# Kernel tuning notes

Measured on AMD Instinct MI355X. Metric: run time of the kernel, lower is better.

## Reference

```python
import jax, jax.numpy as jnp
import numpy as np

N = 50000        # nodes
E = 1_600_000    # edges (avg degree 32)
IN = 512         # in_size
OUT = 512        # out_size
H = 8            # num_heads
D = OUT // H     # head_dim = 64


def setup_inputs() -> dict:
    key = jax.random.key(0)
    ks = jax.random.split(key, 9)
    w_scale = 0.02
    h = jax.random.normal(ks[0], (N, IN), dtype=jnp.float32)
    Wq = jax.random.normal(ks[1], (IN, OUT), dtype=jnp.float32) * w_scale
    bq = jnp.zeros((OUT,), dtype=jnp.float32)
    Wk = jax.random.normal(ks[2], (IN, OUT), dtype=jnp.float32) * w_scale
    bk = jnp.zeros((OUT,), dtype=jnp.float32)
    Wv = jax.random.normal(ks[3], (IN, OUT), dtype=jnp.float32) * w_scale
    bv = jnp.zeros((OUT,), dtype=jnp.float32)
    row = jax.random.randint(ks[4], (E,), 0, N)  # dst node of each edge
    col = jax.random.randint(ks[5], (E,), 0, N)  # src node of each edge
    return {"h": h, "Wq": Wq, "bq": bq, "Wk": Wk, "bk": bk, "Wv": Wv, "bv": bv, "row": row, "col": col}


def reference(h, Wq, bq, Wk, bk, Wv, bv, row, col):
    n = h.shape[0]
    scaling = D ** -0.5
    # prep_qkv: Linear projections, reshape to [N, head_dim, num_heads], scale q
    q = ((h @ Wq) + bq).reshape(n, D, H) * scaling
    k = ((h @ Wk) + bk).reshape(n, D, H)
    v = ((h @ Wv) + bv).reshape(n, D, H)
    # bsddmm: per-nonzero batched dot product, scores[e,h] = <q[row[e],:,h], k[col[e],:,h]>
    scores = jnp.einsum('edh,edh->eh', q[row], k[col])  # [E, H]
    # sparse row-wise softmax over neighbors of each dst node
    m = jax.lax.stop_gradient(jax.ops.segment_max(scores, row, num_segments=n))  # [N, H]
    ex = jnp.exp(scores - m[row])                                                # [E, H]
    denom = jax.ops.segment_sum(ex, row, num_segments=n)                         # [N, H]
    attn = ex / denom[row]                                                       # [E, H]
    # bspmm: out[i,d,h] = sum_{e: row[e]=i} attn[e,h] * v[col[e],d,h]
    out = jax.ops.segment_sum(attn[:, None, :] * v[col], row, num_segments=n)    # [N, D, H]
    return out
```

## Files before the change

kernel.cpp:

```cpp
#include <hip/hip_runtime.h>
#include <hip/hip_bf16.h>
#include <math.h>


#define IN_DIM 512
#define OUT_DIM 512
#define NHEAD 8
#define HDIM 64
#define BM 128
#define BN 128
#define BK 32

typedef short bf16x8 __attribute__((ext_vector_type(8)));
typedef float f32x4 __attribute__((ext_vector_type(4)));
typedef unsigned short ushort8_t __attribute__((ext_vector_type(8)));

__device__ __forceinline__ unsigned short f2bf(float f) {
  union { float f; unsigned int u; } v; v.f = f;
  unsigned int u = v.u;
  u = (u + 0x7FFF + ((u >> 16) & 1)) >> 16;
  return (unsigned short)u;
}
__device__ __forceinline__ float bf2f(unsigned short s) {
  union { unsigned int u; float f; } v; v.u = ((unsigned int)s) << 16;
  return v.f;
}
__device__ __forceinline__ void gload_lds16(const void* g, void* l) {
  __builtin_amdgcn_global_load_lds(
      (const __attribute__((address_space(1))) unsigned int*)g,
      (__attribute__((address_space(3))) unsigned int*)l, 16, 0, 0);
}

__global__ __launch_bounds__(256) void convert_h(const float* __restrict__ Hm,
                                                 unsigned short* __restrict__ hb,
                                                 int Nn) {
  const size_t base = ((size_t)blockIdx.x * blockDim.x + threadIdx.x) * 8;
  const int row = (int)(base >> 9);
  ushort8_t o = {0,0,0,0,0,0,0,0};
  if (row < Nn) {
    const float4 a = *(const float4*)(Hm + base);
    const float4 b = *(const float4*)(Hm + base + 4);
    o[0]=f2bf(a.x); o[1]=f2bf(a.y); o[2]=f2bf(a.z); o[3]=f2bf(a.w);
    o[4]=f2bf(b.x); o[5]=f2bf(b.y); o[6]=f2bf(b.z); o[7]=f2bf(b.w);
  }
  *(ushort8_t*)(hb + base) = o;
}

__global__ __launch_bounds__(256) void convert_w(const float* __restrict__ Wq,
                                                 const float* __restrict__ Wk,
                                                 const float* __restrict__ Wv,
                                                 unsigned short* __restrict__ Wt) {
  __shared__ unsigned short tile[64][72];
  const int mat = blockIdx.z;
  const float* W = (mat == 0) ? Wq : (mat == 1) ? Wk : Wv;
  const int k0 = blockIdx.x * 64, n0 = blockIdx.y * 64;
  const int tid = threadIdx.x;
  const int r = tid >> 2, cb = (tid & 3) * 16;
  #pragma unroll
  for (int x = 0; x < 16; x += 4) {
    const float4 f = *(const float4*)(W + (size_t)(k0 + r) * OUT_DIM + n0 + cb + x);
    tile[cb + x + 0][r] = f2bf(f.x);
    tile[cb + x + 1][r] = f2bf(f.y);
    tile[cb + x + 2][r] = f2bf(f.z);
    tile[cb + x + 3][r] = f2bf(f.w);
  }
  __syncthreads();
  ushort8_t o1, o2;
  #pragma unroll
  for (int x = 0; x < 8; ++x) { o1[x] = tile[r][cb + x]; o2[x] = tile[r][cb + 8 + x]; }
  const int n = n0 + r;
  const int np = ((n & 7) << 6) | (n >> 3);
  unsigned short* dst = Wt + (size_t)(mat * 512 + np) * IN_DIM + k0 + cb;
  *(ushort8_t*)(dst) = o1;
  *(ushort8_t*)(dst + 8) = o2;
}

__global__ __launch_bounds__(256, 2) void qkv_gemm_mfma(
    const unsigned short* __restrict__ hb,
    const unsigned short* __restrict__ Wt,
    const float* __restrict__ bq, const float* __restrict__ bk, const float* __restrict__ bv,
    unsigned short* __restrict__ qTb, unsigned short* __restrict__ kTb,
    unsigned short* __restrict__ vTb, int Nn) {
  __shared__ __align__(16) unsigned short As[BM * BK];
  __shared__ __align__(16) unsigned short Bs[BN * BK];
  const int tid = threadIdx.x;
  const int l = tid & 63;
  const int w = tid >> 6;
  const int wr = w >> 1, wc = w & 1;
  const int row0 = blockIdx.x * BM;
  const int col0 = blockIdx.y * BN;

  const int kcl = tid & 3;
  const int rl0 = tid >> 2;

  for (int mat = 0; mat < 3; ++mat) {
    const unsigned short* Bsrc = Wt + (size_t)(mat * 512 + col0) * IN_DIM;
    f32x4 acc[4][4];
    const f32x4 zero = {0.f, 0.f, 0.f, 0.f};
    #pragma unroll
    for (int m = 0; m < 4; ++m)
      #pragma unroll
      for (int n = 0; n < 4; ++n) acc[m][n] = zero;

    for (int k0 = 0; k0 < IN_DIM; k0 += BK) {
      __syncthreads();
      #pragma unroll
      for (int t = 0; t < 2; ++t) {
        const int rl = rl0 + t * 64;
        const int kk = (kcl ^ ((rl >> 1) & 3)) * 8;
        gload_lds16(hb + (size_t)(row0 + rl) * IN_DIM + k0 + kk,
                    (char*)As + t * 4096 + w * 1024);
        gload_lds16(Bsrc + (size_t)rl * IN_DIM + k0 + kk,
                    (char*)Bs + t * 4096 + w * 1024);
      }
      __syncthreads();
      bf16x8 af[4], bfr[4];
      #pragma unroll
      for (int m = 0; m < 4; ++m) {
        const int row = wr * 64 + m * 16 + (l & 15);
        const int kc = (l >> 4) ^ ((row >> 1) & 3);
        af[m] = *(const bf16x8*)&As[row * BK + kc * 8];
      }
      #pragma unroll
      for (int n = 0; n < 4; ++n) {
        const int row = wc * 64 + n * 16 + (l & 15);
        const int kc = (l >> 4) ^ ((row >> 1) & 3);
        bfr[n] = *(const bf16x8*)&Bs[row * BK + kc * 8];
      }
      #pragma unroll
      for (int m = 0; m < 4; ++m)
        #pragma unroll
        for (int n = 0; n < 4; ++n)
          acc[m][n] = __builtin_amdgcn_mfma_f32_16x16x32_bf16(af[m], bfr[n], acc[m][n], 0, 0, 0);
    }

    const float scale = (mat == 0) ? 0.125f : 1.0f;
    const float* bias = (mat == 0) ? bq : (mat == 1) ? bk : bv;
    unsigned short* dst = (mat == 0) ? qTb : (mat == 1) ? kTb : vTb;
    #pragma unroll
    for (int n = 0; n < 4; ++n) {
      const int cc = col0 + wc * 64 + n * 16 + (l & 15);
      const int o = ((cc & 63) << 3) | (cc >> 6);
      const float bsv = bias[o];
      #pragma unroll
      for (int m = 0; m < 4; ++m) {
        #pragma unroll
        for (int j = 0; j < 4; ++j) {
          const int r = row0 + wr * 64 + m * 16 + (l >> 4) * 4 + j;
          if (r < Nn) dst[(size_t)r * OUT_DIM + cc] = f2bf((acc[m][n][j] + bsv) * scale);
        }
      }
    }
  }
}

__global__ void hist_kernel(const int* __restrict__ row, int* __restrict__ counts, int E_) {
  const int i = blockIdx.x * blockDim.x + threadIdx.x;
  if (i < E_) atomicAdd(&counts[row[i]], 1);
}

__global__ __launch_bounds__(1024) void scan_kernel(const int* __restrict__ counts,
                                                    int* __restrict__ offsets,
                                                    int* __restrict__ cursor, int n) {
  __shared__ int lds[1024];
  __shared__ int running_s;
  const int t = threadIdx.x;
  if (t == 0) running_s = 0;
  __syncthreads();
  for (int base = 0; base < n; base += 1024) {
    const int i = base + t;
    const int c = (i < n) ? counts[i] : 0;
    lds[t] = c;
    __syncthreads();
    int val = c;
    for (int off = 1; off < 1024; off <<= 1) {
      const int add = (t >= off) ? lds[t - off] : 0;
      __syncthreads();
      val += add;
      lds[t] = val;
      __syncthreads();
    }
    const int running = running_s;
    if (i < n) { const int ex = running + val - c; offsets[i] = ex; cursor[i] = ex; }
    __syncthreads();
    if (t == 1023) running_s = running + val;
    __syncthreads();
  }
  if (t == 0) offsets[n] = running_s;
}

__global__ void scatter_kernel(const int* __restrict__ row, const int* __restrict__ col,
                               int* __restrict__ cursor, int* __restrict__ colsorted, int E_) {
  const int i = blockIdx.x * blockDim.x + threadIdx.x;
  if (i < E_) {
    const int pos = atomicAdd(&cursor[row[i]], 1);
    colsorted[pos] = col[i];
  }
}

__global__ __launch_bounds__(256) void bsddmm_node(
    const unsigned short* __restrict__ qb, const unsigned short* __restrict__ kb,
    const int* __restrict__ colsorted, const int* __restrict__ offsets,
    float* __restrict__ scores, float* __restrict__ nodemax, int Nn) {
  const int wid = (int)((blockIdx.x * (size_t)blockDim.x + threadIdx.x) >> 6);
  if (wid >= Nn) return;
  const int l = threadIdx.x & 63;
  const int hh = l >> 3, j = l & 7;
  const int start = offsets[wid], end = offsets[wid + 1];
  if (start == end) return;

  const size_t loff = (size_t)l * 8;
  const ushort8_t q8 = *(const ushort8_t*)(qb + (size_t)wid * OUT_DIM + loff);
  float qf[8];
  #pragma unroll
  for (int x = 0; x < 8; ++x) qf[x] = bf2f(q8[x]);

  float m_run = -1e30f;

  for (int base = start; base < end; base += 64) {
    const int cnt = min(64, end - base);
    const int myc = (l < cnt) ? colsorted[base + l] : 0;
    int u = 0;
    for (; u + 4 <= cnt; u += 4) {
      const int c0 = __shfl(myc, u + 0);
      const int c1 = __shfl(myc, u + 1);
      const int c2 = __shfl(myc, u + 2);
      const int c3 = __shfl(myc, u + 3);
      const ushort8_t ka = *(const ushort8_t*)(kb + (size_t)c0 * OUT_DIM + loff);
      const ushort8_t kb1 = *(const ushort8_t*)(kb + (size_t)c1 * OUT_DIM + loff);
      const ushort8_t kc = *(const ushort8_t*)(kb + (size_t)c2 * OUT_DIM + loff);
      const ushort8_t kd = *(const ushort8_t*)(kb + (size_t)c3 * OUT_DIM + loff);
      float s0 = 0.f, s1 = 0.f, s2 = 0.f, s3 = 0.f;
      #pragma unroll
      for (int x = 0; x < 8; ++x) {
        s0 = fmaf(qf[x], bf2f(ka[x]), s0);
        s1 = fmaf(qf[x], bf2f(kb1[x]), s1);
        s2 = fmaf(qf[x], bf2f(kc[x]), s2);
        s3 = fmaf(qf[x], bf2f(kd[x]), s3);
      }
      s0 += __shfl_xor(s0, 1); s0 += __shfl_xor(s0, 2); s0 += __shfl_xor(s0, 4);
      s1 += __shfl_xor(s1, 1); s1 += __shfl_xor(s1, 2); s1 += __shfl_xor(s1, 4);
      s2 += __shfl_xor(s2, 1); s2 += __shfl_xor(s2, 2); s2 += __shfl_xor(s2, 4);
      s3 += __shfl_xor(s3, 1); s3 += __shfl_xor(s3, 2); s3 += __shfl_xor(s3, 4);
      m_run = fmaxf(m_run, fmaxf(fmaxf(s0, s1), fmaxf(s2, s3)));
      if (j == 0) {
        scores[(size_t)(base + u + 0) * NHEAD + hh] = s0;
        scores[(size_t)(base + u + 1) * NHEAD + hh] = s1;
        scores[(size_t)(base + u + 2) * NHEAD + hh] = s2;
        scores[(size_t)(base + u + 3) * NHEAD + hh] = s3;
      }
    }
    for (; u < cnt; ++u) {
      const int c = __shfl(myc, u);
      const ushort8_t kv = *(const ushort8_t*)(kb + (size_t)c * OUT_DIM + loff);
      float s = 0.f;
      #pragma unroll
      for (int x = 0; x < 8; ++x) s = fmaf(qf[x], bf2f(kv[x]), s);
      s += __shfl_xor(s, 1); s += __shfl_xor(s, 2); s += __shfl_xor(s, 4);
      m_run = fmaxf(m_run, s);
      if (j == 0) scores[(size_t)(base + u) * NHEAD + hh] = s;
    }
  }
  if (j == 0) nodemax[(size_t)wid * NHEAD + hh] = m_run;
}

__device__ __forceinline__ float sel8(const float v[8], int idx) {
  float r = v[0];
  r = (idx == 1) ? v[1] : r;
  r = (idx == 2) ? v[2] : r;
  r = (idx == 3) ? v[3] : r;
  r = (idx == 4) ? v[4] : r;
  r = (idx == 5) ? v[5] : r;
  r = (idx == 6) ? v[6] : r;
  r = (idx == 7) ? v[7] : r;
  return r;
}

__global__ __launch_bounds__(256) void softmax_spmm_kernel(
    const float* __restrict__ scores, const float* __restrict__ nodemax,
    const unsigned short* __restrict__ vb,
    const int* __restrict__ colsorted, const int* __restrict__ offsets,
    float* __restrict__ out, int Nn) {
  const int wid = (int)((blockIdx.x * (size_t)blockDim.x + threadIdx.x) >> 6);
  if (wid >= Nn) return;
  const int l = threadIdx.x & 63;
  const int hh = l >> 3;
  const int dg = (l & 7) * 8;
  const int start = offsets[wid], end = offsets[wid + 1];

  if (start == end) {
    #pragma unroll
    for (int x = 0; x < 8; ++x)
      out[(size_t)wid * OUT_DIM + (size_t)(dg + x) * NHEAD + hh] = 0.f;
    return;
  }

  const float4 ma = *(const float4*)(nodemax + (size_t)wid * NHEAD);
  const float4 mb = *(const float4*)(nodemax + (size_t)wid * NHEAD + 4);
  const float m[8] = {ma.x, ma.y, ma.z, ma.w, mb.x, mb.y, mb.z, mb.w};

  float dsum[8];
  #pragma unroll
  for (int x = 0; x < 8; ++x) dsum[x] = 0.f;
  for (int s = start + l; s < end; s += 64) {
    const float4 a = *(const float4*)(scores + (size_t)s * NHEAD);
    const float4 b = *(const float4*)(scores + (size_t)s * NHEAD + 4);
    dsum[0] += __expf(a.x - m[0]); dsum[1] += __expf(a.y - m[1]);
    dsum[2] += __expf(a.z - m[2]); dsum[3] += __expf(a.w - m[3]);
    dsum[4] += __expf(b.x - m[4]); dsum[5] += __expf(b.y - m[5]);
    dsum[6] += __expf(b.z - m[6]); dsum[7] += __expf(b.w - m[7]);
  }
  #pragma unroll
  for (int off = 1; off < 64; off <<= 1) {
    #pragma unroll
    for (int x = 0; x < 8; ++x) dsum[x] += __shfl_xor(dsum[x], off);
  }

  const float mh  = sel8(m, hh);
  const float inv = 1.0f / sel8(dsum, hh);

  float acc[8];
  #pragma unroll
  for (int x = 0; x < 8; ++x) acc[x] = 0.f;
  const size_t loff = (size_t)l * 8;
  for (int base = start; base < end; base += 64) {
    const int cnt = min(64, end - base);
    const int myc = (l < cnt) ? colsorted[base + l] : 0;
    int u = 0;
    for (; u + 4 <= cnt; u += 4) {
      const int c0 = __shfl(myc, u + 0);
      const int c1 = __shfl(myc, u + 1);
      const int c2 = __shfl(myc, u + 2);
      const int c3 = __shfl(myc, u + 3);
      const float e0 = __expf(scores[(size_t)(base + u + 0) * NHEAD + hh] - mh);
      const float e1 = __expf(scores[(size_t)(base + u + 1) * NHEAD + hh] - mh);
      const float e2 = __expf(scores[(size_t)(base + u + 2) * NHEAD + hh] - mh);
      const float e3 = __expf(scores[(size_t)(base + u + 3) * NHEAD + hh] - mh);
      const ushort8_t va = *(const ushort8_t*)(vb + (size_t)c0 * OUT_DIM + loff);
      const ushort8_t vb1 = *(const ushort8_t*)(vb + (size_t)c1 * OUT_DIM + loff);
      const ushort8_t vc = *(const ushort8_t*)(vb + (size_t)c2 * OUT_DIM + loff);
      const ushort8_t vd = *(const ushort8_t*)(vb + (size_t)c3 * OUT_DIM + loff);
      #pragma unroll
      for (int x = 0; x < 8; ++x) {
        acc[x] = fmaf(e0, bf2f(va[x]), acc[x]);
        acc[x] = fmaf(e1, bf2f(vb1[x]), acc[x]);
        acc[x] = fmaf(e2, bf2f(vc[x]), acc[x]);
        acc[x] = fmaf(e3, bf2f(vd[x]), acc[x]);
      }
    }
    for (; u < cnt; ++u) {
      const int c = __shfl(myc, u);
      const float e = __expf(scores[(size_t)(base + u) * NHEAD + hh] - mh);
      const ushort8_t vv = *(const ushort8_t*)(vb + (size_t)c * OUT_DIM + loff);
      #pragma unroll
      for (int x = 0; x < 8; ++x) acc[x] = fmaf(e, bf2f(vv[x]), acc[x]);
    }
  }
  #pragma unroll
  for (int x = 0; x < 8; ++x)
    out[(size_t)wid * OUT_DIM + (size_t)(dg + x) * NHEAD + hh] = acc[x] * inv;
}

extern "C" void kernel_launch(void* const* d_in, const int* in_sizes, int n_in,
                              void* d_out, int out_size, void* d_ws, size_t ws_size,
                              hipStream_t stream) {
  const float* Hm = (const float*)d_in[0];
  const float* Wq = (const float*)d_in[1];
  const float* bq = (const float*)d_in[2];
  const float* Wk = (const float*)d_in[3];
  const float* bk = (const float*)d_in[4];
  const float* Wv = (const float*)d_in[5];
  const float* bv = (const float*)d_in[6];
  const int* row  = (const int*)d_in[7];
  const int* col  = (const int*)d_in[8];
  float* out = (float*)d_out;

  const int Nn = in_sizes[0] / IN_DIM;
  const int E  = in_sizes[7];
  const int mtiles = (Nn + BM - 1) / BM;
  const int Mpad = mtiles * BM;

  unsigned short* hb  = (unsigned short*)d_ws;
  unsigned short* Wt  = hb + (size_t)Mpad * IN_DIM;
  unsigned short* qTb = Wt + (size_t)3 * 512 * IN_DIM;
  unsigned short* kTb = qTb + (size_t)Nn * OUT_DIM;
  unsigned short* vTb = kTb + (size_t)Nn * OUT_DIM;
  float* scores   = (float*)(vTb + (size_t)Nn * OUT_DIM);
  float* nodemax  = scores + (size_t)E * NHEAD;
  int* counts     = (int*)(nodemax + (size_t)Nn * NHEAD);
  int* offsets    = counts + Nn;
  int* cursor     = offsets + Nn + 1;
  int* colsorted  = cursor + Nn;

  hipMemsetAsync(counts, 0, (size_t)Nn * sizeof(int), stream);
  hist_kernel<<<(E + 255) / 256, 256, 0, stream>>>(row, counts, E);
  scan_kernel<<<1, 1024, 0, stream>>>(counts, offsets, cursor, Nn);
  scatter_kernel<<<(E + 255) / 256, 256, 0, stream>>>(row, col, cursor, colsorted, E);

  const int hblocks = (int)(((size_t)Mpad * IN_DIM / 8 + 255) / 256);
  convert_h<<<hblocks, 256, 0, stream>>>(Hm, hb, Nn);
  convert_w<<<dim3(8, 8, 3), 256, 0, stream>>>(Wq, Wk, Wv, Wt);

  qkv_gemm_mfma<<<dim3(mtiles, 4), 256, 0, stream>>>(hb, Wt, bq, bk, bv,
                                                     qTb, kTb, vTb, Nn);

  const size_t node_threads = (size_t)Nn * 64;
  bsddmm_node<<<(int)((node_threads + 255) / 256), 256, 0, stream>>>(
      qTb, kTb, colsorted, offsets, scores, nodemax, Nn);

  softmax_spmm_kernel<<<(int)((node_threads + 255) / 256), 256, 0, stream>>>(
      scores, nodemax, vTb, colsorted, offsets, out, Nn);
}
```

Measured before the change: 1.129 ms.

## Fuse SDDMM, softmax and SpMM per node with LDS scores; parallelize scan

Merges the score computation, the row softmax and the value aggregation into one kernel. Each wavefront keeps its node's scores in shared memory when the degree is at most 128, so the global scores and nodemax round trips go away, and each score is exponentiated once. Nodes with higher degree fall back to a global scratch path. The single-block sequential prefix scan is replaced by a three-kernel multi-block scan, which removes a serial bottleneck at the cost of two extra launches. The fused kernel uses 16KB of LDS per block, which may limit occupancy.

```diff
diff --git a/kernel.cpp b/kernel.cpp
--- a/kernel.cpp
+++ b/kernel.cpp
@@ -10,6 +10,7 @@
 #define BM 128
 #define BN 128
 #define BK 32
+#define SEGCAP 128
 
 typedef short bf16x8 __attribute__((ext_vector_type(8)));
 typedef float f32x4 __attribute__((ext_vector_type(4)));
@@ -159,34 +160,59 @@
   if (i < E_) atomicAdd(&counts[row[i]], 1);
 }
 
-__global__ __launch_bounds__(1024) void scan_kernel(const int* __restrict__ counts,
-                                                    int* __restrict__ offsets,
-                                                    int* __restrict__ cursor, int n) {
+__global__ __launch_bounds__(256) void scan_partial(const int* __restrict__ counts,
+                                                    int* __restrict__ bsums, int n) {
+  __shared__ int red[256];
+  const int t = threadIdx.x;
+  const int i = blockIdx.x * 256 + t;
+  red[t] = (i < n) ? counts[i] : 0;
+  __syncthreads();
+  #pragma unroll
+  for (int off = 128; off > 0; off >>= 1) {
+    if (t < off) red[t] += red[t + off];
+    __syncthreads();
+  }
+  if (t == 0) bsums[blockIdx.x] = red[0];
+}
+
+__global__ __launch_bounds__(1024) void scan_bsums(int* __restrict__ bsums, int nb) {
   __shared__ int lds[1024];
-  __shared__ int running_s;
   const int t = threadIdx.x;
-  if (t == 0) running_s = 0;
+  const int v = (t < nb) ? bsums[t] : 0;
+  lds[t] = v;
   __syncthreads();
-  for (int base = 0; base < n; base += 1024) {
-    const int i = base + t;
-    const int c = (i < n) ? counts[i] : 0;
-    lds[t] = c;
+  for (int off = 1; off < 1024; off <<= 1) {
+    const int add = (t >= off) ? lds[t - off] : 0;
     __syncthreads();
-    int val = c;
-    for (int off = 1; off < 1024; off <<= 1) {
-      const int add = (t >= off) ? lds[t - off] : 0;
-      __syncthreads();
-      val += add;
-      lds[t] = val;
-      __syncthreads();
-    }
-    const int running = running_s;
-    if (i < n) { const int ex = running + val - c; offsets[i] = ex; cursor[i] = ex; }
+    lds[t] += add;
     __syncthreads();
-    if (t == 1023) running_s = running + val;
+  }
+  if (t < nb) bsums[t] = lds[t] - v;
+}
+
+__global__ __launch_bounds__(256) void scan_final(const int* __restrict__ counts,
+                                                  const int* __restrict__ bsums,
+                                                  int* __restrict__ offsets,
+                                                  int* __restrict__ cursor,
+                                                  int n, int E_) {
+  __shared__ int lds[256];
+  const int t = threadIdx.x;
+  const int i = blockIdx.x * 256 + t;
+  const int c = (i < n) ? counts[i] : 0;
+  lds[t] = c;
+  __syncthreads();
+  for (int off = 1; off < 256; off <<= 1) {
+    const int add = (t >= off) ? lds[t - off] : 0;
     __syncthreads();
-  }
-  if (t == 0) offsets[n] = running_s;
+    lds[t] += add;
+    __syncthreads();
+  }
+  if (i < n) {
+    const int ex = lds[t] - c + bsums[blockIdx.x];
+    offsets[i] = ex;
+    cursor[i] = ex;
+  }
+  if (blockIdx.x == 0 && t == 0) offsets[n] = E_;
 }
 
 __global__ void scatter_kernel(const int* __restrict__ row, const int* __restrict__ col,
@@ -198,164 +224,173 @@
   }
 }
 
-__global__ __launch_bounds__(256) void bsddmm_node(
+__global__ __launch_bounds__(256) void fused_attn(
     const unsigned short* __restrict__ qb, const unsigned short* __restrict__ kb,
+    const unsigned short* __restrict__ vb,
     const int* __restrict__ colsorted, const int* __restrict__ offsets,
-    float* __restrict__ scores, float* __restrict__ nodemax, int Nn) {
+    float* __restrict__ gscores,
+    float* __restrict__ out, int Nn) {
+  __shared__ float slds_all[4][SEGCAP * NHEAD];
   const int wid = (int)((blockIdx.x * (size_t)blockDim.x + threadIdx.x) >> 6);
   if (wid >= Nn) return;
   const int l = threadIdx.x & 63;
   const int hh = l >> 3, j = l & 7;
   const int start = offsets[wid], end = offsets[wid + 1];
-  if (start == end) return;
-
+  const int seg = end - start;
   const size_t loff = (size_t)l * 8;
-  const ushort8_t q8 = *(const ushort8_t*)(qb + (size_t)wid * OUT_DIM + loff);
-  float qf[8];
-  #pragma unroll
-  for (int x = 0; x < 8; ++x) qf[x] = bf2f(q8[x]);
-
-  float m_run = -1e30f;
-
-  for (int base = start; base < end; base += 64) {
-    const int cnt = min(64, end - base);
-    const int myc = (l < cnt) ? colsorted[base + l] : 0;
-    int u = 0;
-    for (; u + 4 <= cnt; u += 4) {
-      const int c0 = __shfl(myc, u + 0);
-      const int c1 = __shfl(myc, u + 1);
-      const int c2 = __shfl(myc, u + 2);
-      const int c3 = __shfl(myc, u + 3);
-      const ushort8_t ka = *(const ushort8_t*)(kb + (size_t)c0 * OUT_DIM + loff);
-      const ushort8_t kb1 = *(const ushort8_t*)(kb + (size_t)c1 * OUT_DIM + loff);
-      const ushort8_t kc = *(const ushort8_t*)(kb + (size_t)c2 * OUT_DIM + loff);
-      const ushort8_t kd = *(const ushort8_t*)(kb + (size_t)c3 * OUT_DIM + loff);
-      float s0 = 0.f, s1 = 0.f, s2 = 0.f, s3 = 0.f;
-      #pragma unroll
-      for (int x = 0; x < 8; ++x) {
-        s0 = fmaf(qf[x], bf2f(ka[x]), s0);
-        s1 = fmaf(qf[x], bf2f(kb1[x]), s1);
-        s2 = fmaf(qf[x], bf2f(kc[x]), s2);
-        s3 = fmaf(qf[x], bf2f(kd[x]), s3);
-      }
-      s0 += __shfl_xor(s0, 1); s0 += __shfl_xor(s0, 2); s0 += __shfl_xor(s0, 4);
-      s1 += __shfl_xor(s1, 1); s1 += __shfl_xor(s1, 2); s1 += __shfl_xor(s1, 4);
-      s2 += __shfl_xor(s2, 1); s2 += __shfl_xor(s2, 2); s2 += __shfl_xor(s2, 4);
-      s3 += __shfl_xor(s3, 1); s3 += __shfl_xor(s3, 2); s3 += __shfl_xor(s3, 4);
-      m_run = fmaxf(m_run, fmaxf(fmaxf(s0, s1), fmaxf(s2, s3)));
-      if (j == 0) {
-        scores[(size_t)(base + u + 0) * NHEAD + hh] = s0;
-        scores[(size_t)(base + u + 1) * NHEAD + hh] = s1;
-        scores[(size_t)(base + u + 2) * NHEAD + hh] = s2;
-        scores[(size_t)(base + u + 3) * NHEAD + hh] = s3;
-      }
-    }
-    for (; u < cnt; ++u) {
-      const int c = __shfl(myc, u);
-      const ushort8_t kv = *(const ushort8_t*)(kb + (size_t)c * OUT_DIM + loff);
-      float s = 0.f;
-      #pragma unroll
-      for (int x = 0; x < 8; ++x) s = fmaf(qf[x], bf2f(kv[x]), s);
-      s += __shfl_xor(s, 1); s += __shfl_xor(s, 2); s += __shfl_xor(s, 4);
-      m_run = fmaxf(m_run, s);
-      if (j == 0) scores[(size_t)(base + u) * NHEAD + hh] = s;
-    }
-  }
-  if (j == 0) nodemax[(size_t)wid * NHEAD + hh] = m_run;
-}
-
-__device__ __forceinline__ float sel8(const float v[8], int idx) {
-  float r = v[0];
-  r = (idx == 1) ? v[1] : r;
-  r = (idx == 2) ? v[2] : r;
-  r = (idx == 3) ? v[3] : r;
-  r = (idx == 4) ? v[4] : r;
-  r = (idx == 5) ? v[5] : r;
-  r = (idx == 6) ? v[6] : r;
-  r = (idx == 7) ? v[7] : r;
-  return r;
-}
-
-__global__ __launch_bounds__(256) void softmax_spmm_kernel(
-    const float* __restrict__ scores, const float* __restrict__ nodemax,
-    const unsigned short* __restrict__ vb,
-    const int* __restrict__ colsorted, const int* __restrict__ offsets,
-    float* __restrict__ out, int Nn) {
-  const int wid = (int)((blockIdx.x * (size_t)blockDim.x + threadIdx.x) >> 6);
-  if (wid >= Nn) return;
-  const int l = threadIdx.x & 63;
-  const int hh = l >> 3;
   const int dg = (l & 7) * 8;
-  const int start = offsets[wid], end = offsets[wid + 1];
-
-  if (start == end) {
-    #pragma unroll
-    for (int x = 0; x < 8; ++x)
-      out[(size_t)wid * OUT_DIM + (size_t)(dg + x) * NHEAD + hh] = 0.f;
-    return;
-  }
-
-  const float4 ma = *(const float4*)(nodemax + (size_t)wid * NHEAD);
-  const float4 mb = *(const float4*)(nodemax + (size_t)wid * NHEAD + 4);
-  const float m[8] = {ma.x, ma.y, ma.z, ma.w, mb.x, mb.y, mb.z, mb.w};
-
-  float dsum[8];
-  #pragma unroll
-  for (int x = 0; x < 8; ++x) dsum[x] = 0.f;
-  for (int s = start + l; s < end; s += 64) {
-    const float4 a = *(const float4*)(scores + (size_t)s * NHEAD);
-    const float4 b = *(const float4*)(scores + (size_t)s * NHEAD + 4);
-    dsum[0] += __expf(a.x - m[0]); dsum[1] += __expf(a.y - m[1]);
-    dsum[2] += __expf(a.z - m[2]); dsum[3] += __expf(a.w - m[3]);
-    dsum[4] += __expf(b.x - m[4]); dsum[5] += __expf(b.y - m[5]);
-    dsum[6] += __expf(b.z - m[6]); dsum[7] += __expf(b.w - m[7]);
-  }
-  #pragma unroll
-  for (int off = 1; off < 64; off <<= 1) {
-    #pragma unroll
-    for (int x = 0; x < 8; ++x) dsum[x] += __shfl_xor(dsum[x], off);
-  }
-
-  const float mh  = sel8(m, hh);
-  const float inv = 1.0f / sel8(dsum, hh);
 
   float acc[8];
   #pragma unroll
   for (int x = 0; x < 8; ++x) acc[x] = 0.f;
-  const size_t loff = (size_t)l * 8;
-  for (int base = start; base < end; base += 64) {
-    const int cnt = min(64, end - base);
-    const int myc = (l < cnt) ? colsorted[base + l] : 0;
-    int u = 0;
-    for (; u + 4 <= cnt; u += 4) {
-      const int c0 = __shfl(myc, u + 0);
-      const int c1 = __shfl(myc, u + 1);
-      const int c2 = __shfl(myc, u + 2);
-      const int c3 = __shfl(myc, u + 3);
-      const float e0 = __expf(scores[(size_t)(base + u + 0) * NHEAD + hh] - mh);
-      const float e1 = __expf(scores[(size_t)(base + u + 1) * NHEAD + hh] - mh);
-      const float e2 = __expf(scores[(size_t)(base + u + 2) * NHEAD + hh] - mh);
-      const float e3 = __expf(scores[(size_t)(base + u + 3) * NHEAD + hh] - mh);
-      const ushort8_t va = *(const ushort8_t*)(vb + (size_t)c0 * OUT_DIM + loff);
-      const ushort8_t vb1 = *(const ushort8_t*)(vb + (size_t)c1 * OUT_DIM + loff);
-      const ushort8_t vc = *(const ushort8_t*)(vb + (size_t)c2 * OUT_DIM + loff);
-      const ushort8_t vd = *(const ushort8_t*)(vb + (size_t)c3 * OUT_DIM + loff);
-      #pragma unroll
-      for (int x = 0; x < 8; ++x) {
-        acc[x] = fmaf(e0, bf2f(va[x]), acc[x]);
-        acc[x] = fmaf(e1, bf2f(vb1[x]), acc[x]);
-        acc[x] = fmaf(e2, bf2f(vc[x]), acc[x]);
-        acc[x] = fmaf(e3, bf2f(vd[x]), acc[x]);
+  float inv = 0.f;
+
+  if (seg > 0) {
+    const ushort8_t q8 = *(const ushort8_t*)(qb + (size_t)wid * OUT_DIM + loff);
+    float qf[8];
+    #pragma unroll
+    for (int x = 0; x < 8; ++x) qf[x] = bf2f(q8[x]);
+
+    if (seg <= SEGCAP) {
+      float* slds = slds_all[threadIdx.x >> 6];
+      const int myc0 = (l < seg) ? colsorted[start + l] : 0;
+      const int myc1 = (64 + l < seg) ? colsorted[start + 64 + l] : 0;
+      float m_run = -1e30f;
+
+      #pragma unroll
+      for (int chunk = 0; chunk < 2; ++chunk) {
+        const int base = chunk * 64;
+        if (base >= seg) break;
+        const int cnt = min(64, seg - base);
+        const int myc = chunk ? myc1 : myc0;
+        int u = 0;
+        for (; u + 4 <= cnt; u += 4) {
+          const int c0 = __shfl(myc, u + 0);
+          const int c1 = __shfl(myc, u + 1);
+          const int c2 = __shfl(myc, u + 2);
+          const int c3 = __shfl(myc, u + 3);
+          const ushort8_t ka = *(const ushort8_t*)(kb + (size_t)c0 * OUT_DIM + loff);
+          const ushort8_t kb1 = *(const ushort8_t*)(kb + (size_t)c1 * OUT_DIM + loff);
+          const ushort8_t kc = *(const ushort8_t*)(kb + (size_t)c2 * OUT_DIM + loff);
+          const ushort8_t kd = *(const ushort8_t*)(kb + (size_t)c3 * OUT_DIM + loff);
+          float s0 = 0.f, s1 = 0.f, s2 = 0.f, s3 = 0.f;
+          #pragma unroll
+          for (int x = 0; x < 8; ++x) {
+            s0 = fmaf(qf[x], bf2f(ka[x]), s0);
+            s1 = fmaf(qf[x], bf2f(kb1[x]), s1);
+            s2 = fmaf(qf[x], bf2f(kc[x]), s2);
+            s3 = fmaf(qf[x], bf2f(kd[x]), s3);
+          }
+          s0 += __shfl_xor(s0, 1); s0 += __shfl_xor(s0, 2); s0 += __shfl_xor(s0, 4);
+          s1 += __shfl_xor(s1, 1); s1 += __shfl_xor(s1, 2); s1 += __shfl_xor(s1, 4);
+          s2 += __shfl_xor(s2, 1); s2 += __shfl_xor(s2, 2); s2 += __shfl_xor(s2, 4);
+          s3 += __shfl_xor(s3, 1); s3 += __shfl_xor(s3, 2); s3 += __shfl_xor(s3, 4);
+          m_run = fmaxf(m_run, fmaxf(fmaxf(s0, s1), fmaxf(s2, s3)));
+          if (j == 0) {
+            slds[(base + u + 0) * NHEAD + hh] = s0;
+            slds[(base + u + 1) * NHEAD + hh] = s1;
+            slds[(base + u + 2) * NHEAD + hh] = s2;
+            slds[(base + u + 3) * NHEAD + hh] = s3;
+          }
+        }
+        for (; u < cnt; ++u) {
+          const int c = __shfl(myc, u);
+          const ushort8_t kv = *(const ushort8_t*)(kb + (size_t)c * OUT_DIM + loff);
+          float s = 0.f;
+          #pragma unroll
+          for (int x = 0; x < 8; ++x) s = fmaf(qf[x], bf2f(kv[x]), s);
+          s += __shfl_xor(s, 1); s += __shfl_xor(s, 2); s += __shfl_xor(s, 4);
+          m_run = fmaxf(m_run, s);
+          if (j == 0) slds[(base + u) * NHEAD + hh] = s;
+        }
+      }
+      __builtin_amdgcn_wave_barrier();
+
+      float dsum = 0.f;
+      for (int u = j; u < seg; u += 8) {
+        const float ex = __expf(slds[u * NHEAD + hh] - m_run);
+        slds[u * NHEAD + hh] = ex;
+        dsum += ex;
+      }
+      dsum += __shfl_xor(dsum, 1);
+      dsum += __shfl_xor(dsum, 2);
+      dsum += __shfl_xor(dsum, 4);
+      inv = 1.0f / dsum;
+      __builtin_amdgcn_wave_barrier();
+
+      #pragma unroll
+      for (int chunk = 0; chunk < 2; ++chunk) {
+        const int base = chunk * 64;
+        if (base >= seg) break;
+        const int cnt = min(64, seg - base);
+        const int myc = chunk ? myc1 : myc0;
+        int u = 0;
+        for (; u + 4 <= cnt; u += 4) {
+          const int c0 = __shfl(myc, u + 0);
+          const int c1 = __shfl(myc, u + 1);
+          const int c2 = __shfl(myc, u + 2);
+          const int c3 = __shfl(myc, u + 3);
+          const float e0 = slds[(base + u + 0) * NHEAD + hh];
+          const float e1 = slds[(base + u + 1) * NHEAD + hh];
+          const float e2 = slds[(base + u + 2) * NHEAD + hh];
+          const float e3 = slds[(base + u + 3) * NHEAD + hh];
+          const ushort8_t va = *(const ushort8_t*)(vb + (size_t)c0 * OUT_DIM + loff);
+          const ushort8_t vb1 = *(const ushort8_t*)(vb + (size_t)c1 * OUT_DIM + loff);
+          const ushort8_t vc = *(const ushort8_t*)(vb + (size_t)c2 * OUT_DIM + loff);
+          const ushort8_t vd = *(const ushort8_t*)(vb + (size_t)c3 * OUT_DIM + loff);
+          #pragma unroll
+          for (int x = 0; x < 8; ++x) {
+            acc[x] = fmaf(e0, bf2f(va[x]), acc[x]);
+            acc[x] = fmaf(e1, bf2f(vb1[x]), acc[x]);
+            acc[x] = fmaf(e2, bf2f(vc[x]), acc[x]);
+            acc[x] = fmaf(e3, bf2f(vd[x]), acc[x]);
+          }
+        }
+        for (; u < cnt; ++u) {
+          const int c = __shfl(myc, u);
+          const float e = slds[(base + u) * NHEAD + hh];
+          const ushort8_t vv = *(const ushort8_t*)(vb + (size_t)c * OUT_DIM + loff);
+          #pragma unroll
+          for (int x = 0; x < 8; ++x) acc[x] = fmaf(e, bf2f(vv[x]), acc[x]);
+        }
+      }
+    } else {
+      float m_run = -1e30f;
+      for (int base = start; base < end; base += 64) {
+        const int cnt = min(64, end - base);
+        const int myc = (l < cnt) ? colsorted[base + l] : 0;
+        for (int u = 0; u < cnt; ++u) {
+          const int c = __shfl(myc, u);
+          const ushort8_t kv = *(const ushort8_t*)(kb + (size_t)c * OUT_DIM + loff);
+          float s = 0.f;
+          #pragma unroll
+          for (int x = 0; x < 8; ++x) s = fmaf(qf[x], bf2f(kv[x]), s);
+          s += __shfl_xor(s, 1); s += __shfl_xor(s, 2); s += __shfl_xor(s, 4);
+          m_run = fmaxf(m_run, s);
+          if (j == 0) gscores[(size_t)(base + u) * NHEAD + hh] = s;
+        }
+      }
+      float dsum = 0.f;
+      for (int e = start + j; e < end; e += 8)
+        dsum += __expf(gscores[(size_t)e * NHEAD + hh] - m_run);
+      dsum += __shfl_xor(dsum, 1);
+      dsum += __shfl_xor(dsum, 2);
+      dsum += __shfl_xor(dsum, 4);
+      inv = 1.0f / dsum;
+      for (int base = start; base < end; base += 64) {
+        const int cnt = min(64, end - base);
+        const int myc = (l < cnt) ? colsorted[base + l] : 0;
+        for (int u = 0; u < cnt; ++u) {
+          const int c = __shfl(myc, u);
+          const float e = __expf(gscores[(size_t)(base + u) * NHEAD + hh] - m_run);
+          const ushort8_t vv = *(const ushort8_t*)(vb + (size_t)c * OUT_DIM + loff);
+          #pragma unroll
+          for (int x = 0; x < 8; ++x) acc[x] = fmaf(e, bf2f(vv[x]), acc[x]);
+        }
       }
     }
-    for (; u < cnt; ++u) {
-      const int c = __shfl(myc, u);
-      const float e = __expf(scores[(size_t)(base + u) * NHEAD + hh] - mh);
-      const ushort8_t vv = *(const ushort8_t*)(vb + (size_t)c * OUT_DIM + loff);
-      #pragma unroll
-      for (int x = 0; x < 8; ++x) acc[x] = fmaf(e, bf2f(vv[x]), acc[x]);
-    }
-  }
+  }
+
   #pragma unroll
   for (int x = 0; x < 8; ++x)
     out[(size_t)wid * OUT_DIM + (size_t)(dg + x) * NHEAD + hh] = acc[x] * inv;
@@ -379,22 +414,25 @@
   const int E  = in_sizes[7];
   const int mtiles = (Nn + BM - 1) / BM;
   const int Mpad = mtiles * BM;
+  const int nb = (Nn + 255) / 256;
 
   unsigned short* hb  = (unsigned short*)d_ws;
   unsigned short* Wt  = hb + (size_t)Mpad * IN_DIM;
   unsigned short* qTb = Wt + (size_t)3 * 512 * IN_DIM;
   unsigned short* kTb = qTb + (size_t)Nn * OUT_DIM;
   unsigned short* vTb = kTb + (size_t)Nn * OUT_DIM;
-  float* scores   = (float*)(vTb + (size_t)Nn * OUT_DIM);
-  float* nodemax  = scores + (size_t)E * NHEAD;
-  int* counts     = (int*)(nodemax + (size_t)Nn * NHEAD);
+  float* gscores  = (float*)(vTb + (size_t)Nn * OUT_DIM);
+  int* counts     = (int*)(gscores + (size_t)E * NHEAD);
   int* offsets    = counts + Nn;
   int* cursor     = offsets + Nn + 1;
   int* colsorted  = cursor + Nn;
+  int* bsums      = colsorted + E;
 
   hipMemsetAsync(counts, 0, (size_t)Nn * sizeof(int), stream);
   hist_kernel<<<(E + 255) / 256, 256, 0, stream>>>(row, counts, E);
-  scan_kernel<<<1, 1024, 0, stream>>>(counts, offsets, cursor, Nn);
+  scan_partial<<<nb, 256, 0, stream>>>(counts, bsums, Nn);
+  scan_bsums<<<1, 1024, 0, stream>>>(bsums, nb);
+  scan_final<<<nb, 256, 0, stream>>>(counts, bsums, offsets, cursor, Nn, E);
   scatter_kernel<<<(E + 255) / 256, 256, 0, stream>>>(row, col, cursor, colsorted, E);
 
   const int hblocks = (int)(((size_t)Mpad * IN_DIM / 8 + 255) / 256);
@@ -405,9 +443,6 @@
                                                      qTb, kTb, vTb, Nn);
 
   const size_t node_threads = (size_t)Nn * 64;
-  bsddmm_node<<<(int)((node_threads + 255) / 256), 256, 0, stream>>>(
-      qTb, kTb, colsorted, offsets, scores, nodemax, Nn);
-
-  softmax_spmm_kernel<<<(int)((node_threads + 255) / 256), 256, 0, stream>>>(
-      scores, nodemax, vTb, colsorted, offsets, out, Nn);
-}
+  fused_attn<<<(int)((node_threads + 255) / 256), 256, 0, stream>>>(
+      qTb, kTb, vTb, colsorted, offsets, gscores, out, Nn);
+}
```

New measurement: 1.049 ms. 1.08x faster.
